# Performance work log

Hardware: AMD Instinct MI355X
Metric: run time of the kernel (lower is better)

## Reference

```python
import jax, jax.numpy as jnp
import numpy as np

N_NODES = 50000
N_EDGES = 800000
IN_CH = 128
HID = 64
HEADS = 4
OUT_CH = 1
NEG_SLOPE = 0.2  # PyG GATConv default


def setup_inputs() -> dict:
    key = jax.random.key(0)
    ks = jax.random.split(key, 16)
    s = 0.1
    x = jax.random.normal(ks[0], (N_NODES, IN_CH), dtype=jnp.float32)
    edge_index = jax.random.randint(ks[1], (2, N_EDGES), 0, N_NODES, dtype=jnp.int64)
    # GATConv 1: in=128 -> 64 per head, 4 heads, concat
    W1 = jax.random.normal(ks[2], (IN_CH, HEADS * HID), dtype=jnp.float32) * s
    att_src1 = jax.random.normal(ks[3], (HEADS, HID), dtype=jnp.float32) * s
    att_dst1 = jax.random.normal(ks[4], (HEADS, HID), dtype=jnp.float32) * s
    b1 = jnp.zeros((HEADS * HID,), dtype=jnp.float32)
    # GATConv 2: in=256 -> 64, 1 head, mean (concat=False)
    W2 = jax.random.normal(ks[5], (HEADS * HID, HID), dtype=jnp.float32) * s
    att_src2 = jax.random.normal(ks[6], (1, HID), dtype=jnp.float32) * s
    att_dst2 = jax.random.normal(ks[7], (1, HID), dtype=jnp.float32) * s
    b2 = jnp.zeros((HID,), dtype=jnp.float32)
    # MLP: Linear(128,64) -> ReLU -> Linear(64,1)
    mlp_w1 = jax.random.normal(ks[8], (2 * HID, HID), dtype=jnp.float32) * s
    mlp_b1 = jnp.zeros((HID,), dtype=jnp.float32)
    mlp_w2 = jax.random.normal(ks[9], (HID, OUT_CH), dtype=jnp.float32) * s
    mlp_b2 = jnp.zeros((OUT_CH,), dtype=jnp.float32)
    return dict(x=x, edge_index=edge_index, W1=W1, att_src1=att_src1,
                att_dst1=att_dst1, b1=b1, W2=W2, att_src2=att_src2,
                att_dst2=att_dst2, b2=b2, mlp_w1=mlp_w1, mlp_b1=mlp_b1,
                mlp_w2=mlp_w2, mlp_b2=mlp_b2)


def gat_layer(x, edge_index, W, att_src, att_dst, bias, heads, ch, concat):
    N = x.shape[0]
    # add self loops (PyG default add_self_loops=True)
    loop = jnp.arange(N, dtype=edge_index.dtype)
    src = jnp.concatenate([edge_index[0], loop])
    dst = jnp.concatenate([edge_index[1], loop])
    h = (x @ W).reshape(N, heads, ch)                      # [N,H,C]
    a_src = jnp.einsum('nhc,hc->nh', h, att_src)           # [N,H]
    a_dst = jnp.einsum('nhc,hc->nh', h, att_dst)
    logits = jax.nn.leaky_relu(a_src[src] + a_dst[dst], NEG_SLOPE)  # [E,H]
    # segment softmax over destination node
    m = jax.ops.segment_max(logits, dst, num_segments=N)
    e = jnp.exp(logits - m[dst])
    denom = jax.ops.segment_sum(e, dst, num_segments=N)
    alpha = e / denom[dst]                                 # [E,H]
    msg = alpha[:, :, None] * h[src]                       # [E,H,C]
    out = jax.ops.segment_sum(msg, dst, num_segments=N)    # [N,H,C]
    out = out.reshape(N, heads * ch) if concat else out.mean(axis=1)
    return out + bias


def reference(x, edge_index, W1, att_src1, att_dst1, b1,
              W2, att_src2, att_dst2, b2,
              mlp_w1, mlp_b1, mlp_w2, mlp_b2):
    # eval mode: dropouts are identity
    h = gat_layer(x, edge_index, W1, att_src1, att_dst1, b1, HEADS, HID, True)
    h = jax.nn.elu(h)
    h = gat_layer(h, edge_index, W2, att_src2, att_dst2, b2, 1, HID, False)
    u = h[edge_index[0]]                                   # [E,HID]
    v = h[edge_index[1]]
    ef = jnp.concatenate([u, v], axis=1)                   # [E,2*HID]
    hid = jax.nn.relu(ef @ mlp_w1 + mlp_b1)
    return hid @ mlp_w2 + mlp_b2                           # [E,OUT_CH]
```

## Files before the change

### kernel.cpp

```cpp
#include <hip/hip_runtime.h>
#include <hip/hip_bf16.h>
#include <math.h>

#define NN 50000
#define NE 800000
#define ET (NE + NN)
#define NB ((NN + 255) / 256)
#define NEG 0.2f

typedef __hip_bfloat16 bf16;
typedef __attribute__((ext_vector_type(8))) short s8v;
typedef __attribute__((ext_vector_type(4))) float f4v;

__device__ __forceinline__ float bf2f(unsigned short u) {
  union { unsigned int i; float f; } c;
  c.i = ((unsigned int)u) << 16;
  return c.f;
}
__device__ __forceinline__ unsigned short f2b(float f) {
  bf16 b = __float2bfloat16(f);
  return __builtin_bit_cast(unsigned short, b);
}

__global__ void zero_counts_k(int* __restrict__ c) {
  int i = blockIdx.x * 256 + threadIdx.x;
  if (i < NN) c[i] = 0;
}

__global__ void hist_k(const int* __restrict__ ei, int* __restrict__ counts) {
  int e = blockIdx.x * 256 + threadIdx.x;
  if (e >= ET) return;
  int d = (e < NE) ? ei[NE + e] : (e - NE);
  atomicAdd(&counts[d], 1);
}

__global__ __launch_bounds__(256) void scan_bsum_k(const int* __restrict__ counts,
                                                   int* __restrict__ bsums) {
  __shared__ int wsum[4];
  int i = blockIdx.x * 256 + threadIdx.x;
  int v = (i < NN) ? counts[i] : 0;
#pragma unroll
  for (int off = 32; off; off >>= 1) v += __shfl_xor(v, off);
  if ((threadIdx.x & 63) == 0) wsum[threadIdx.x >> 6] = v;
  __syncthreads();
  if (threadIdx.x == 0) bsums[blockIdx.x] = wsum[0] + wsum[1] + wsum[2] + wsum[3];
}

__global__ __launch_bounds__(256) void scan_top_k(int* __restrict__ bsums) {
  __shared__ int s[256];
  int t = threadIdx.x;
  int v = (t < NB) ? bsums[t] : 0;
  s[t] = v;
  __syncthreads();
  for (int off = 1; off < 256; off <<= 1) {
    int u = (t >= off) ? s[t - off] : 0;
    __syncthreads();
    s[t] += u;
    __syncthreads();
  }
  if (t < NB) bsums[t] = s[t] - v;
}

__global__ __launch_bounds__(256) void scan_final_k(const int* __restrict__ counts,
                                                    const int* __restrict__ bsums,
                                                    int* __restrict__ offsets,
                                                    int* __restrict__ cursor) {
  __shared__ int s[256];
  int t = threadIdx.x;
  int i = blockIdx.x * 256 + t;
  int v = (i < NN) ? counts[i] : 0;
  s[t] = v;
  __syncthreads();
  for (int off = 1; off < 256; off <<= 1) {
    int u = (t >= off) ? s[t - off] : 0;
    __syncthreads();
    s[t] += u;
    __syncthreads();
  }
  int excl = s[t] - v + bsums[blockIdx.x];
  if (i < NN) {
    offsets[i] = excl;
    cursor[i] = excl;
    if (i == NN - 1) offsets[NN] = excl + v;
  }
}

__global__ void scatter_k(const int* __restrict__ ei, int* __restrict__ cursor,
                          int* __restrict__ csr) {
  int e = blockIdx.x * 256 + threadIdx.x;
  if (e >= ET) return;
  int s, d;
  if (e < NE) { s = ei[e]; d = ei[NE + e]; } else { s = e - NE; d = s; }
  int pos = atomicAdd(&cursor[d], 1);
  csr[pos] = s;
}

__global__ void convx_k(const float* __restrict__ in, unsigned short* __restrict__ out,
                        int n4) {
  int i = blockIdx.x * 256 + threadIdx.x;
  if (i >= n4) return;
  float4 v = *(const float4*)(in + (size_t)i * 4);
  ushort4 o = {f2b(v.x), f2b(v.y), f2b(v.z), f2b(v.w)};
  *(ushort4*)(out + (size_t)i * 4) = o;
}

__global__ void convT_k(const float* __restrict__ in, unsigned short* __restrict__ out,
                        int K, int N) {
  int i = blockIdx.x * 256 + threadIdx.x;
  if (i >= K * N) return;
  int n = i / K, k = i - n * K;
  out[i] = f2b(in[(size_t)k * N + n]);
}

__global__ void convPQ_k(const float* __restrict__ mw1, unsigned short* __restrict__ out) {
  int i = blockIdx.x * 256 + threadIdx.x;
  if (i >= 128 * 64) return;
  int n = i >> 6, k = i & 63;
  float v = (n < 64) ? mw1[(size_t)k * 64 + n] : mw1[(size_t)(64 + k) * 64 + (n - 64)];
  out[i] = f2b(v);
}

template <int DOTS>
__global__ __launch_bounds__(256) void mgemm_k(
    const unsigned short* __restrict__ A, int lda,
    const unsigned short* __restrict__ Bt, int ldb,
    unsigned short* __restrict__ C, int ldc,
    int M, int N, int K,
    const float* __restrict__ ws, const float* __restrict__ wd,
    float* __restrict__ as_, float* __restrict__ ad_, int H) {
  __shared__ unsigned short Asl[64][40];
  __shared__ unsigned short Btl[64][40];
  __shared__ float sdot[64], ddot[64];
  int bm = blockIdx.y * 64, bn = blockIdx.x * 64;
  int t = threadIdx.x;
  int wv = t >> 6, lane = t & 63;
  int wm = (wv >> 1) * 32, wn = (wv & 1) * 32;
  int l16 = lane & 15, lq = lane >> 4;
  if (DOTS && t < 64) { sdot[t] = 0.f; ddot[t] = 0.f; }
  f4v acc[2][2];
#pragma unroll
  for (int mi = 0; mi < 2; ++mi)
#pragma unroll
    for (int ni = 0; ni < 2; ++ni) {
      acc[mi][ni][0] = 0.f; acc[mi][ni][1] = 0.f;
      acc[mi][ni][2] = 0.f; acc[mi][ni][3] = 0.f;
    }
  int sr = t >> 2, sc = (t & 3) * 8;
  for (int k0 = 0; k0 < K; k0 += 32) {
    uint4 av = {0, 0, 0, 0};
    int gr = bm + sr;
    if (gr < M) av = *(const uint4*)(A + (size_t)gr * lda + k0 + sc);
    *(uint4*)&Asl[sr][sc] = av;
    uint4 bv = *(const uint4*)(Bt + (size_t)(bn + sr) * ldb + k0 + sc);
    *(uint4*)&Btl[sr][sc] = bv;
    __syncthreads();
    s8v af[2], bfv[2];
#pragma unroll
    for (int mi = 0; mi < 2; ++mi)
      af[mi] = *(const s8v*)&Asl[wm + mi * 16 + l16][lq * 8];
#pragma unroll
    for (int ni = 0; ni < 2; ++ni)
      bfv[ni] = *(const s8v*)&Btl[wn + ni * 16 + l16][lq * 8];
#pragma unroll
    for (int mi = 0; mi < 2; ++mi)
#pragma unroll
      for (int ni = 0; ni < 2; ++ni)
        acc[mi][ni] = __builtin_amdgcn_mfma_f32_16x16x32_bf16(
            af[mi], bfv[ni], acc[mi][ni], 0, 0, 0);
    __syncthreads();
  }
#pragma unroll
  for (int mi = 0; mi < 2; ++mi)
#pragma unroll
    for (int rr = 0; rr < 4; ++rr) {
      int row = bm + wm + mi * 16 + lq * 4 + rr;
      if (row < M) {
#pragma unroll
        for (int ni = 0; ni < 2; ++ni) {
          int col = bn + wn + ni * 16 + l16;
          C[(size_t)row * ldc + col] = f2b(acc[mi][ni][rr]);
        }
      }
    }
  if (DOTS) {
    int head = blockIdx.x;
    float ps[2][4], pd[2][4];
#pragma unroll
    for (int mi = 0; mi < 2; ++mi)
#pragma unroll
      for (int rr = 0; rr < 4; ++rr) {
        float s = 0.f, d = 0.f;
#pragma unroll
        for (int ni = 0; ni < 2; ++ni) {
          int col = wn + ni * 16 + l16;
          s += acc[mi][ni][rr] * ws[head * 64 + col];
          d += acc[mi][ni][rr] * wd[head * 64 + col];
        }
        ps[mi][rr] = s;
        pd[mi][rr] = d;
      }
#pragma unroll
    for (int off = 1; off < 16; off <<= 1)
#pragma unroll
      for (int mi = 0; mi < 2; ++mi)
#pragma unroll
        for (int rr = 0; rr < 4; ++rr) {
          ps[mi][rr] += __shfl_xor(ps[mi][rr], off);
          pd[mi][rr] += __shfl_xor(pd[mi][rr], off);
        }
    if (l16 == 0) {
#pragma unroll
      for (int mi = 0; mi < 2; ++mi)
#pragma unroll
        for (int rr = 0; rr < 4; ++rr) {
          int rl = wm + mi * 16 + lq * 4 + rr;
          atomicAdd(&sdot[rl], ps[mi][rr]);
          atomicAdd(&ddot[rl], pd[mi][rr]);
        }
    }
    __syncthreads();
    if (t < 64 && bm + t < M) {
      as_[(size_t)(bm + t) * H + head] = sdot[t];
      ad_[(size_t)(bm + t) * H + head] = ddot[t];
    }
  }
}

__global__ __launch_bounds__(256) void gat_agg4_k(
    const int* __restrict__ offsets, const int* __restrict__ csr,
    const unsigned short* __restrict__ h, const float* __restrict__ as_,
    const float* __restrict__ ad_, const float* __restrict__ bias,
    unsigned short* __restrict__ out) {
  __shared__ float exs[4][64][4];
  __shared__ int srcs[4][64];
  int wv = threadIdx.x >> 6, lane = threadIdx.x & 63;
  int n = blockIdx.x * 4 + wv;
  int hd = lane >> 4;
  int beg = offsets[n], end = offsets[n + 1];
  float4 adn = *(const float4*)(ad_ + (size_t)n * 4);
  float m0 = -1e30f, m1 = -1e30f, m2 = -1e30f, m3 = -1e30f;
  float d0 = 0.f, d1 = 0.f, d2 = 0.f, d3 = 0.f;
  float4 acc = {0.f, 0.f, 0.f, 0.f};
  for (int base = beg; base < end; base += 64) {
    int cnt = min(64, end - base);
    int src = 0;
    float l0 = -1e30f, l1 = -1e30f, l2 = -1e30f, l3 = -1e30f;
    if (lane < cnt) {
      src = csr[base + lane];
      float4 a4 = *(const float4*)(as_ + (size_t)src * 4);
      float t;
      t = a4.x + adn.x; l0 = (t > 0.f) ? t : NEG * t;
      t = a4.y + adn.y; l1 = (t > 0.f) ? t : NEG * t;
      t = a4.z + adn.z; l2 = (t > 0.f) ? t : NEG * t;
      t = a4.w + adn.w; l3 = (t > 0.f) ? t : NEG * t;
    }
    float t0 = l0, t1 = l1, t2 = l2, t3 = l3;
#pragma unroll
    for (int off = 32; off; off >>= 1) {
      t0 = fmaxf(t0, __shfl_xor(t0, off));
      t1 = fmaxf(t1, __shfl_xor(t1, off));
      t2 = fmaxf(t2, __shfl_xor(t2, off));
      t3 = fmaxf(t3, __shfl_xor(t3, off));
    }
    float M0 = fmaxf(m0, t0), M1 = fmaxf(m1, t1), M2 = fmaxf(m2, t2), M3 = fmaxf(m3, t3);
    float e0 = 0.f, e1 = 0.f, e2 = 0.f, e3 = 0.f;
    if (lane < cnt) {
      e0 = __expf(l0 - M0); e1 = __expf(l1 - M1);
      e2 = __expf(l2 - M2); e3 = __expf(l3 - M3);
    }
    float s0 = e0, s1 = e1, s2 = e2, s3 = e3;
#pragma unroll
    for (int off = 32; off; off >>= 1) {
      s0 += __shfl_xor(s0, off);
      s1 += __shfl_xor(s1, off);
      s2 += __shfl_xor(s2, off);
      s3 += __shfl_xor(s3, off);
    }
    float sc0 = __expf(m0 - M0), sc1 = __expf(m1 - M1);
    float sc2 = __expf(m2 - M2), sc3 = __expf(m3 - M3);
    d0 = d0 * sc0 + s0; d1 = d1 * sc1 + s1;
    d2 = d2 * sc2 + s2; d3 = d3 * sc3 + s3;
    m0 = M0; m1 = M1; m2 = M2; m3 = M3;
    float mysc = (hd == 0) ? sc0 : (hd == 1) ? sc1 : (hd == 2) ? sc2 : sc3;
    acc.x *= mysc; acc.y *= mysc; acc.z *= mysc; acc.w *= mysc;
    float4 ex4 = {e0, e1, e2, e3};
    *(float4*)(&exs[wv][lane][0]) = ex4;
    srcs[wv][lane] = src;
    __builtin_amdgcn_wave_barrier();
    int e = 0;
    for (; e + 4 <= cnt; e += 4) {
      int si0 = srcs[wv][e], si1 = srcs[wv][e + 1];
      int si2 = srcs[wv][e + 2], si3 = srcs[wv][e + 3];
      float w0 = exs[wv][e][hd], w1 = exs[wv][e + 1][hd];
      float w2 = exs[wv][e + 2][hd], w3 = exs[wv][e + 3][hd];
      ushort4 r0 = *(const ushort4*)(h + (size_t)si0 * 256 + lane * 4);
      ushort4 r1 = *(const ushort4*)(h + (size_t)si1 * 256 + lane * 4);
      ushort4 r2 = *(const ushort4*)(h + (size_t)si2 * 256 + lane * 4);
      ushort4 r3 = *(const ushort4*)(h + (size_t)si3 * 256 + lane * 4);
      acc.x += w0 * bf2f(r0.x); acc.y += w0 * bf2f(r0.y);
      acc.z += w0 * bf2f(r0.z); acc.w += w0 * bf2f(r0.w);
      acc.x += w1 * bf2f(r1.x); acc.y += w1 * bf2f(r1.y);
      acc.z += w1 * bf2f(r1.z); acc.w += w1 * bf2f(r1.w);
      acc.x += w2 * bf2f(r2.x); acc.y += w2 * bf2f(r2.y);
      acc.z += w2 * bf2f(r2.z); acc.w += w2 * bf2f(r2.w);
      acc.x += w3 * bf2f(r3.x); acc.y += w3 * bf2f(r3.y);
      acc.z += w3 * bf2f(r3.z); acc.w += w3 * bf2f(r3.w);
    }
    for (; e < cnt; ++e) {
      int si = srcs[wv][e];
      float w = exs[wv][e][hd];
      ushort4 r = *(const ushort4*)(h + (size_t)si * 256 + lane * 4);
      acc.x += w * bf2f(r.x); acc.y += w * bf2f(r.y);
      acc.z += w * bf2f(r.z); acc.w += w * bf2f(r.w);
    }
  }
  float myden = (hd == 0) ? d0 : (hd == 1) ? d1 : (hd == 2) ? d2 : d3;
  float4 b4 = *(const float4*)(bias + lane * 4);
  float4 res;
  res.x = acc.x / myden + b4.x;
  res.y = acc.y / myden + b4.y;
  res.z = acc.z / myden + b4.z;
  res.w = acc.w / myden + b4.w;
  res.x = (res.x > 0.f) ? res.x : (__expf(res.x) - 1.f);
  res.y = (res.y > 0.f) ? res.y : (__expf(res.y) - 1.f);
  res.z = (res.z > 0.f) ? res.z : (__expf(res.z) - 1.f);
  res.w = (res.w > 0.f) ? res.w : (__expf(res.w) - 1.f);
  ushort4 ov = {f2b(res.x), f2b(res.y), f2b(res.z), f2b(res.w)};
  *(ushort4*)(out + (size_t)n * 256 + lane * 4) = ov;
}

__global__ __launch_bounds__(256) void gat_agg1_k(
    const int* __restrict__ offsets, const int* __restrict__ csr,
    const unsigned short* __restrict__ h, const float* __restrict__ as_,
    const float* __restrict__ ad_, const float* __restrict__ bias,
    unsigned short* __restrict__ out) {
  __shared__ float exs[4][64];
  __shared__ int srcs[4][64];
  int wv = threadIdx.x >> 6, lane = threadIdx.x & 63;
  int n = blockIdx.x * 4 + wv;
  int slot = lane >> 5, cp = lane & 31;
  int beg = offsets[n], end = offsets[n + 1];
  float adn = ad_[n];
  float m = -1e30f, den = 0.f;
  float ax = 0.f, ay = 0.f;
  for (int base = beg; base < end; base += 64) {
    int cnt = min(64, end - base);
    int src = 0;
    float l = -1e30f;
    if (lane < cnt) {
      src = csr[base + lane];
      float t = as_[src] + adn;
      l = (t > 0.f) ? t : NEG * t;
    }
    float mt = l;
#pragma unroll
    for (int off = 32; off; off >>= 1) mt = fmaxf(mt, __shfl_xor(mt, off));
    float M = fmaxf(m, mt);
    float ex = (lane < cnt) ? __expf(l - M) : 0.f;
    float s = ex;
#pragma unroll
    for (int off = 32; off; off >>= 1) s += __shfl_xor(s, off);
    float sc = __expf(m - M);
    den = den * sc + s;
    m = M;
    ax *= sc; ay *= sc;
    exs[wv][lane] = ex;
    srcs[wv][lane] = src;
    __builtin_amdgcn_wave_barrier();
    int e = 0;
    for (; e + 8 <= cnt; e += 8) {
      int i0 = e + slot, i1 = e + 2 + slot, i2 = e + 4 + slot, i3 = e + 6 + slot;
      int si0 = srcs[wv][i0], si1 = srcs[wv][i1], si2 = srcs[wv][i2], si3 = srcs[wv][i3];
      float w0 = exs[wv][i0], w1 = exs[wv][i1], w2 = exs[wv][i2], w3 = exs[wv][i3];
      ushort2 r0 = *(const ushort2*)(h + (size_t)si0 * 64 + cp * 2);
      ushort2 r1 = *(const ushort2*)(h + (size_t)si1 * 64 + cp * 2);
      ushort2 r2 = *(const ushort2*)(h + (size_t)si2 * 64 + cp * 2);
      ushort2 r3 = *(const ushort2*)(h + (size_t)si3 * 64 + cp * 2);
      ax += w0 * bf2f(r0.x); ay += w0 * bf2f(r0.y);
      ax += w1 * bf2f(r1.x); ay += w1 * bf2f(r1.y);
      ax += w2 * bf2f(r2.x); ay += w2 * bf2f(r2.y);
      ax += w3 * bf2f(r3.x); ay += w3 * bf2f(r3.y);
    }
    for (; e < cnt; e += 2) {
      int i = e + slot;
      int ok = (i < cnt);
      int si = srcs[wv][ok ? i : 0];
      float w = ok ? exs[wv][i] : 0.f;
      ushort2 r = *(const ushort2*)(h + (size_t)si * 64 + cp * 2);
      ax += w * bf2f(r.x); ay += w * bf2f(r.y);
    }
  }
  ax += __shfl_xor(ax, 32);
  ay += __shfl_xor(ay, 32);
  if (slot == 0) {
    ushort2 ov;
    ov.x = f2b(ax / den + bias[cp * 2]);
    ov.y = f2b(ay / den + bias[cp * 2 + 1]);
    *(ushort2*)(out + (size_t)n * 64 + cp * 2) = ov;
  }
}

__global__ __launch_bounds__(256) void edge_out_k(
    const int* __restrict__ ei, const unsigned short* __restrict__ pq,
    const float* __restrict__ mb1, const float* __restrict__ w2,
    const float* __restrict__ mb2, float* __restrict__ out) {
  int wid = blockIdx.x * 4 + (threadIdx.x >> 6);
  int lane = threadIdx.x & 63;
  int slot = lane >> 5, cp = lane & 31;
  int e = wid * 2 + slot;
  if (e >= NE) return;
  int s = ei[e], d = ei[NE + e];
  ushort2 rp = *(const ushort2*)(pq + (size_t)s * 128 + cp * 2);
  ushort2 rq = *(const ushort2*)(pq + (size_t)d * 128 + 64 + cp * 2);
  float2 mb = *(const float2*)(mb1 + cp * 2);
  float2 wv2 = *(const float2*)(w2 + cp * 2);
  float v0 = bf2f(rp.x) + bf2f(rq.x) + mb.x;
  float v1 = bf2f(rp.y) + bf2f(rq.y) + mb.y;
  v0 = fmaxf(v0, 0.f);
  v1 = fmaxf(v1, 0.f);
  float r = v0 * wv2.x + v1 * wv2.y;
#pragma unroll
  for (int off = 16; off; off >>= 1) r += __shfl_xor(r, off);
  if (cp == 0) out[e] = r + mb2[0];
}

extern "C" void kernel_launch(void* const* d_in, const int* in_sizes, int n_in,
                              void* d_out, int out_size, void* d_ws, size_t ws_size,
                              hipStream_t stream) {
  const float* x = (const float*)d_in[0];
  const int* ei = (const int*)d_in[1];
  const float* W1 = (const float*)d_in[2];
  const float* as1w = (const float*)d_in[3];
  const float* ad1w = (const float*)d_in[4];
  const float* b1 = (const float*)d_in[5];
  const float* W2 = (const float*)d_in[6];
  const float* as2w = (const float*)d_in[7];
  const float* ad2w = (const float*)d_in[8];
  const float* b2 = (const float*)d_in[9];
  const float* mw1 = (const float*)d_in[10];
  const float* mb1 = (const float*)d_in[11];
  const float* mw2 = (const float*)d_in[12];
  const float* mb2 = (const float*)d_in[13];
  float* out = (float*)d_out;

  char* ws = (char*)d_ws;
  size_t o = 0;
  auto alloc = [&](size_t bytes) {
    void* ptr = ws + o;
    o += (bytes + 255) & ~(size_t)255;
    return ptr;
  };
  int* counts = (int*)alloc((size_t)NN * 4);
  int* offsets = (int*)alloc((size_t)(NN + 1) * 4);
  int* cursor = (int*)alloc((size_t)NN * 4);
  int* bsums = (int*)alloc((size_t)NB * 4);
  int* csr = (int*)alloc((size_t)ET * 4);
  unsigned short* xb = (unsigned short*)alloc((size_t)NN * 128 * 2);
  unsigned short* w1t = (unsigned short*)alloc((size_t)256 * 128 * 2);
  unsigned short* w2t = (unsigned short*)alloc((size_t)64 * 256 * 2);
  unsigned short* pqt = (unsigned short*)alloc((size_t)128 * 64 * 2);
  unsigned short* h1b = (unsigned short*)alloc((size_t)NN * 256 * 2);
  float* a_s1 = (float*)alloc((size_t)NN * 4 * 4);
  float* a_d1 = (float*)alloc((size_t)NN * 4 * 4);
  unsigned short* x2b = (unsigned short*)alloc((size_t)NN * 256 * 2);
  unsigned short* yb = (unsigned short*)alloc((size_t)NN * 64 * 2);
  unsigned short* h2b = h1b;
  unsigned short* pq = h1b + (size_t)NN * 64;

  zero_counts_k<<<NB, 256, 0, stream>>>(counts);
  hist_k<<<(ET + 255) / 256, 256, 0, stream>>>(ei, counts);
  scan_bsum_k<<<NB, 256, 0, stream>>>(counts, bsums);
  scan_top_k<<<1, 256, 0, stream>>>(bsums);
  scan_final_k<<<NB, 256, 0, stream>>>(counts, bsums, offsets, cursor);
  scatter_k<<<(ET + 255) / 256, 256, 0, stream>>>(ei, cursor, csr);

  convx_k<<<(NN * 32 + 255) / 256, 256, 0, stream>>>(x, xb, NN * 32);
  convT_k<<<(256 * 128 + 255) / 256, 256, 0, stream>>>(W1, w1t, 128, 256);
  convT_k<<<(64 * 256 + 255) / 256, 256, 0, stream>>>(W2, w2t, 256, 64);
  convPQ_k<<<(128 * 64 + 255) / 256, 256, 0, stream>>>(mw1, pqt);

  int gy = (NN + 63) / 64;
  mgemm_k<1><<<dim3(4, gy), 256, 0, stream>>>(xb, 128, w1t, 128, h1b, 256,
                                              NN, 256, 128, as1w, ad1w, a_s1, a_d1, 4);
  gat_agg4_k<<<NN / 4, 256, 0, stream>>>(offsets, csr, h1b, a_s1, a_d1, b1, x2b);

  mgemm_k<1><<<dim3(1, gy), 256, 0, stream>>>(x2b, 256, w2t, 256, h2b, 64,
                                              NN, 64, 256, as2w, ad2w, a_s1, a_d1, 1);
  gat_agg1_k<<<NN / 4, 256, 0, stream>>>(offsets, csr, h2b, a_s1, a_d1, b2, yb);

  mgemm_k<0><<<dim3(2, gy), 256, 0, stream>>>(yb, 64, pqt, 64, pq, 128,
                                              NN, 128, 64, nullptr, nullptr,
                                              nullptr, nullptr, 0);

  edge_out_k<<<(NE / 2 + 3) / 4, 256, 0, stream>>>(ei, pq, mb1, mw2, mb2, out);
}
```

Baseline: 327.1 us.

## Store edge ids in CSR and run edge MLP per destination node

The CSR array now holds (src, edge_id) pairs, so the final edge MLP kernel can walk each destination node's incoming edges. Each node's q-row and bias are then loaded once and reused, and output is scattered by the original edge id. The 4-head aggregation inner loop also widens from 4 to 8 gathers in flight. The cost is a doubled CSR footprint read by both GAT aggregation kernels, plus scattered output writes and idle lanes on low-degree nodes in the edge kernel.

Result: faster. 307.2 us (-6.1%).

```diff
diff --git a/kernel.cpp b/kernel.cpp
--- a/kernel.cpp
+++ b/kernel.cpp
@@ -86,13 +86,14 @@
 }
 
 __global__ void scatter_k(const int* __restrict__ ei, int* __restrict__ cursor,
-                          int* __restrict__ csr) {
+                          int2* __restrict__ csr) {
   int e = blockIdx.x * 256 + threadIdx.x;
   if (e >= ET) return;
-  int s, d;
-  if (e < NE) { s = ei[e]; d = ei[NE + e]; } else { s = e - NE; d = s; }
+  int s, d, id;
+  if (e < NE) { s = ei[e]; d = ei[NE + e]; id = e; }
+  else { s = e - NE; d = s; id = -1; }
   int pos = atomicAdd(&cursor[d], 1);
-  csr[pos] = s;
+  csr[pos] = make_int2(s, id);
 }
 
 __global__ void convx_k(const float* __restrict__ in, unsigned short* __restrict__ out,
@@ -227,14 +228,14 @@
 }
 
 __global__ __launch_bounds__(256) void gat_agg4_k(
-    const int* __restrict__ offsets, const int* __restrict__ csr,
+    const int* __restrict__ offsets, const int2* __restrict__ csr,
     const unsigned short* __restrict__ h, const float* __restrict__ as_,
     const float* __restrict__ ad_, const float* __restrict__ bias,
     unsigned short* __restrict__ out) {
   __shared__ float exs[4][64][4];
   __shared__ int srcs[4][64];
-  int wv = threadIdx.x >> 6, lane = threadIdx.x & 63;
-  int n = blockIdx.x * 4 + wv;
+  int wvx = threadIdx.x >> 6, lane = threadIdx.x & 63;
+  int n = blockIdx.x * 4 + wvx;
   int hd = lane >> 4;
   int beg = offsets[n], end = offsets[n + 1];
   float4 adn = *(const float4*)(ad_ + (size_t)n * 4);
@@ -246,7 +247,7 @@
     int src = 0;
     float l0 = -1e30f, l1 = -1e30f, l2 = -1e30f, l3 = -1e30f;
     if (lane < cnt) {
-      src = csr[base + lane];
+      src = csr[base + lane].x;
       float4 a4 = *(const float4*)(as_ + (size_t)src * 4);
       float t;
       t = a4.x + adn.x; l0 = (t > 0.f) ? t : NEG * t;
@@ -284,31 +285,28 @@
     float mysc = (hd == 0) ? sc0 : (hd == 1) ? sc1 : (hd == 2) ? sc2 : sc3;
     acc.x *= mysc; acc.y *= mysc; acc.z *= mysc; acc.w *= mysc;
     float4 ex4 = {e0, e1, e2, e3};
-    *(float4*)(&exs[wv][lane][0]) = ex4;
-    srcs[wv][lane] = src;
+    *(float4*)(&exs[wvx][lane][0]) = ex4;
+    srcs[wvx][lane] = src;
     __builtin_amdgcn_wave_barrier();
     int e = 0;
-    for (; e + 4 <= cnt; e += 4) {
-      int si0 = srcs[wv][e], si1 = srcs[wv][e + 1];
-      int si2 = srcs[wv][e + 2], si3 = srcs[wv][e + 3];
-      float w0 = exs[wv][e][hd], w1 = exs[wv][e + 1][hd];
-      float w2 = exs[wv][e + 2][hd], w3 = exs[wv][e + 3][hd];
-      ushort4 r0 = *(const ushort4*)(h + (size_t)si0 * 256 + lane * 4);
-      ushort4 r1 = *(const ushort4*)(h + (size_t)si1 * 256 + lane * 4);
-      ushort4 r2 = *(const ushort4*)(h + (size_t)si2 * 256 + lane * 4);
-      ushort4 r3 = *(const ushort4*)(h + (size_t)si3 * 256 + lane * 4);
-      acc.x += w0 * bf2f(r0.x); acc.y += w0 * bf2f(r0.y);
-      acc.z += w0 * bf2f(r0.z); acc.w += w0 * bf2f(r0.w);
-      acc.x += w1 * bf2f(r1.x); acc.y += w1 * bf2f(r1.y);
-      acc.z += w1 * bf2f(r1.z); acc.w += w1 * bf2f(r1.w);
-      acc.x += w2 * bf2f(r2.x); acc.y += w2 * bf2f(r2.y);
-      acc.z += w2 * bf2f(r2.z); acc.w += w2 * bf2f(r2.w);
-      acc.x += w3 * bf2f(r3.x); acc.y += w3 * bf2f(r3.y);
-      acc.z += w3 * bf2f(r3.z); acc.w += w3 * bf2f(r3.w);
+    for (; e + 8 <= cnt; e += 8) {
+      ushort4 r[8];
+      float w[8];
+#pragma unroll
+      for (int j = 0; j < 8; ++j) {
+        int si = srcs[wvx][e + j];
+        w[j] = exs[wvx][e + j][hd];
+        r[j] = *(const ushort4*)(h + (size_t)si * 256 + lane * 4);
+      }
+#pragma unroll
+      for (int j = 0; j < 8; ++j) {
+        acc.x += w[j] * bf2f(r[j].x); acc.y += w[j] * bf2f(r[j].y);
+        acc.z += w[j] * bf2f(r[j].z); acc.w += w[j] * bf2f(r[j].w);
+      }
     }
     for (; e < cnt; ++e) {
-      int si = srcs[wv][e];
-      float w = exs[wv][e][hd];
+      int si = srcs[wvx][e];
+      float w = exs[wvx][e][hd];
       ushort4 r = *(const ushort4*)(h + (size_t)si * 256 + lane * 4);
       acc.x += w * bf2f(r.x); acc.y += w * bf2f(r.y);
       acc.z += w * bf2f(r.z); acc.w += w * bf2f(r.w);
@@ -330,14 +328,14 @@
 }
 
 __global__ __launch_bounds__(256) void gat_agg1_k(
-    const int* __restrict__ offsets, const int* __restrict__ csr,
+    const int* __restrict__ offsets, const int2* __restrict__ csr,
     const unsigned short* __restrict__ h, const float* __restrict__ as_,
     const float* __restrict__ ad_, const float* __restrict__ bias,
     unsigned short* __restrict__ out) {
   __shared__ float exs[4][64];
   __shared__ int srcs[4][64];
-  int wv = threadIdx.x >> 6, lane = threadIdx.x & 63;
-  int n = blockIdx.x * 4 + wv;
+  int wvx = threadIdx.x >> 6, lane = threadIdx.x & 63;
+  int n = blockIdx.x * 4 + wvx;
   int slot = lane >> 5, cp = lane & 31;
   int beg = offsets[n], end = offsets[n + 1];
   float adn = ad_[n];
@@ -348,7 +346,7 @@
     int src = 0;
     float l = -1e30f;
     if (lane < cnt) {
-      src = csr[base + lane];
+      src = csr[base + lane].x;
       float t = as_[src] + adn;
       l = (t > 0.f) ? t : NEG * t;
     }
@@ -364,14 +362,14 @@
     den = den * sc + s;
     m = M;
     ax *= sc; ay *= sc;
-    exs[wv][lane] = ex;
-    srcs[wv][lane] = src;
+    exs[wvx][lane] = ex;
+    srcs[wvx][lane] = src;
     __builtin_amdgcn_wave_barrier();
     int e = 0;
     for (; e + 8 <= cnt; e += 8) {
       int i0 = e + slot, i1 = e + 2 + slot, i2 = e + 4 + slot, i3 = e + 6 + slot;
-      int si0 = srcs[wv][i0], si1 = srcs[wv][i1], si2 = srcs[wv][i2], si3 = srcs[wv][i3];
-      float w0 = exs[wv][i0], w1 = exs[wv][i1], w2 = exs[wv][i2], w3 = exs[wv][i3];
+      int si0 = srcs[wvx][i0], si1 = srcs[wvx][i1], si2 = srcs[wvx][i2], si3 = srcs[wvx][i3];
+      float w0 = exs[wvx][i0], w1 = exs[wvx][i1], w2 = exs[wvx][i2], w3 = exs[wvx][i3];
       ushort2 r0 = *(const ushort2*)(h + (size_t)si0 * 64 + cp * 2);
       ushort2 r1 = *(const ushort2*)(h + (size_t)si1 * 64 + cp * 2);
       ushort2 r2 = *(const ushort2*)(h + (size_t)si2 * 64 + cp * 2);
@@ -384,8 +382,8 @@
     for (; e < cnt; e += 2) {
       int i = e + slot;
       int ok = (i < cnt);
-      int si = srcs[wv][ok ? i : 0];
-      float w = ok ? exs[wv][i] : 0.f;
+      int si = srcs[wvx][ok ? i : 0];
+      float w = ok ? exs[wvx][i] : 0.f;
       ushort2 r = *(const ushort2*)(h + (size_t)si * 64 + cp * 2);
       ax += w * bf2f(r.x); ay += w * bf2f(r.y);
     }
@@ -401,27 +399,39 @@
 }
 
 __global__ __launch_bounds__(256) void edge_out_k(
-    const int* __restrict__ ei, const unsigned short* __restrict__ pq,
+    const int* __restrict__ offsets, const int2* __restrict__ csr,
+    const unsigned short* __restrict__ pq,
     const float* __restrict__ mb1, const float* __restrict__ w2,
     const float* __restrict__ mb2, float* __restrict__ out) {
-  int wid = blockIdx.x * 4 + (threadIdx.x >> 6);
-  int lane = threadIdx.x & 63;
-  int slot = lane >> 5, cp = lane & 31;
-  int e = wid * 2 + slot;
-  if (e >= NE) return;
-  int s = ei[e], d = ei[NE + e];
-  ushort2 rp = *(const ushort2*)(pq + (size_t)s * 128 + cp * 2);
-  ushort2 rq = *(const ushort2*)(pq + (size_t)d * 128 + 64 + cp * 2);
-  float2 mb = *(const float2*)(mb1 + cp * 2);
-  float2 wv2 = *(const float2*)(w2 + cp * 2);
-  float v0 = bf2f(rp.x) + bf2f(rq.x) + mb.x;
-  float v1 = bf2f(rp.y) + bf2f(rq.y) + mb.y;
-  v0 = fmaxf(v0, 0.f);
-  v1 = fmaxf(v1, 0.f);
-  float r = v0 * wv2.x + v1 * wv2.y;
-#pragma unroll
-  for (int off = 16; off; off >>= 1) r += __shfl_xor(r, off);
-  if (cp == 0) out[e] = r + mb2[0];
+  int wvx = threadIdx.x >> 6, lane = threadIdx.x & 63;
+  int n = blockIdx.x * 4 + wvx;
+  int slot = lane >> 4, cp = lane & 15;
+  int beg = offsets[n], end = offsets[n + 1];
+  ushort4 qv = *(const ushort4*)(pq + (size_t)n * 128 + 64 + cp * 4);
+  float4 base4 = *(const float4*)(mb1 + cp * 4);
+  base4.x += bf2f(qv.x); base4.y += bf2f(qv.y);
+  base4.z += bf2f(qv.z); base4.w += bf2f(qv.w);
+  float4 w4 = *(const float4*)(w2 + cp * 4);
+  float b2v = mb2[0];
+  for (int base = beg; base < end; base += 4) {
+    int i = base + slot;
+    int2 se = {0, -1};
+    if (i < end) se = csr[i];
+    float r = 0.f;
+    if (se.y >= 0) {
+      ushort4 pv = *(const ushort4*)(pq + (size_t)se.x * 128 + cp * 4);
+      float v0 = fmaxf(bf2f(pv.x) + base4.x, 0.f);
+      float v1 = fmaxf(bf2f(pv.y) + base4.y, 0.f);
+      float v2 = fmaxf(bf2f(pv.z) + base4.z, 0.f);
+      float v3 = fmaxf(bf2f(pv.w) + base4.w, 0.f);
+      r = v0 * w4.x + v1 * w4.y + v2 * w4.z + v3 * w4.w;
+    }
+    r += __shfl_xor(r, 8);
+    r += __shfl_xor(r, 4);
+    r += __shfl_xor(r, 2);
+    r += __shfl_xor(r, 1);
+    if (cp == 0 && se.y >= 0) out[se.y] = r + b2v;
+  }
 }
 
 extern "C" void kernel_launch(void* const* d_in, const int* in_sizes, int n_in,
@@ -454,7 +464,7 @@
   int* offsets = (int*)alloc((size_t)(NN + 1) * 4);
   int* cursor = (int*)alloc((size_t)NN * 4);
   int* bsums = (int*)alloc((size_t)NB * 4);
-  int* csr = (int*)alloc((size_t)ET * 4);
+  int2* csr = (int2*)alloc((size_t)ET * 8);
   unsigned short* xb = (unsigned short*)alloc((size_t)NN * 128 * 2);
   unsigned short* w1t = (unsigned short*)alloc((size_t)256 * 128 * 2);
   unsigned short* w2t = (unsigned short*)alloc((size_t)64 * 256 * 2);
@@ -492,5 +502,5 @@
                                               NN, 128, 64, nullptr, nullptr,
                                               nullptr, nullptr, 0);
 
-  edge_out_k<<<(NE / 2 + 3) / 4, 256, 0, stream>>>(ei, pq, mb1, mw2, mb2, out);
-}
+  edge_out_k<<<NN / 4, 256, 0, stream>>>(offsets, csr, pq, mb1, mw2, mb2, out);
+}
```
